# Kernel optimization log

Hardware: AMD Instinct MI355X
Metric: run time of the kernel (lower is better)

Reference implementation:

```python
import jax, jax.numpy as jnp
import numpy as np

B, T, D, H = 128, 64, 1024, 16
HD = D // H  # head dim = 64, matches smolgen per-pair bias last dim


def setup_inputs() -> dict:
    key = jax.random.key(0)
    ks = jax.random.split(key, 8)
    w = 0.02  # RandomNormal(stddev=0.02) init used throughout the repo
    return {
        "x": jax.random.normal(ks[0], (B, T, D), jnp.float32),
        # per-pair smolgen biases, shared across heads: [B, T, T, head_dim]
        "a_q": jax.random.normal(ks[1], (B, T, T, HD), jnp.float32) * 0.1,
        "a_k": jax.random.normal(ks[2], (B, T, T, HD), jnp.float32) * 0.1,
        "a_v": jax.random.normal(ks[3], (B, T, T, HD), jnp.float32) * 0.1,
        "Wq": jax.random.normal(ks[4], (D, D), jnp.float32) * w,
        "Wk": jax.random.normal(ks[5], (D, D), jnp.float32) * w,
        "Wv": jax.random.normal(ks[6], (D, D), jnp.float32) * w,
        "Wo": jax.random.normal(ks[7], (D, D), jnp.float32) * w,
    }


def reference(x, a_q, a_k, a_v, Wq, Wk, Wv, Wo):
    b, t, d_model = x.shape
    q = (x @ Wq).reshape(b, t, H, HD)
    k = (x @ Wk).reshape(b, t, H, HD)
    v = (x @ Wv).reshape(b, t, H, HD)
    scale = 1.0 / np.sqrt(HD).astype(np.float32)
    # standard content-content logits
    logits = jnp.einsum("bqhd,bkhd->bhqk", q, k) * scale
    # additive per-pair smolgen biases folded into QK^T (broadcast over heads)
    logits = logits + jnp.einsum("bqkd,bkhd->bhqk", a_q, k)
    logits = logits + jnp.einsum("bqhd,bqkd->bhqk", q, a_k)
    probs = jax.nn.softmax(logits, axis=-1)
    out = jnp.einsum("bhqk,bkhd->bqhd", probs, v)
    # per-pair value bias gathered by attention weights
    out = out + jnp.einsum("bhqk,bqkd->bqhd", probs, a_v)
    return out.reshape(b, t, d_model) @ Wo
```

## Files before the change

kernel.cpp:

```cpp
#include <hip/hip_runtime.h>
#include <hip/hip_bf16.h>

#define Bn 128
#define Tn 64
#define Dn 1024
#define Hn 16
#define HDn 64

typedef __bf16 bf16_t;
typedef __bf16 bf16x8 __attribute__((ext_vector_type(8)));
typedef float f32x4 __attribute__((ext_vector_type(4)));

__device__ __forceinline__ f32x4 mfma16(bf16x8 a, bf16x8 b, f32x4 c) {
  return __builtin_amdgcn_mfma_f32_16x16x32_bf16(a, b, c, 0, 0, 0);
}

__device__ __forceinline__ bf16x8 ld8f(const float* p) {
  float4 a = *(const float4*)p;
  float4 b = *(const float4*)(p + 4);
  bf16x8 r;
  r[0] = (bf16_t)a.x; r[1] = (bf16_t)a.y; r[2] = (bf16_t)a.z; r[3] = (bf16_t)a.w;
  r[4] = (bf16_t)b.x; r[5] = (bf16_t)b.y; r[6] = (bf16_t)b.z; r[7] = (bf16_t)b.w;
  return r;
}

__global__ __launch_bounds__(256) void convert_bf16(const float* __restrict__ src,
                                                    bf16_t* __restrict__ dst) {
  long i = ((long)blockIdx.x * 256 + threadIdx.x) * 8;
  *(bf16x8*)(dst + i) = ld8f(src + i);
}

__global__ __launch_bounds__(256) void transpose_mat(const float* __restrict__ W,
                                                     bf16_t* __restrict__ Wt) {
  __shared__ bf16_t tile[64][65];
  const int tr = blockIdx.y, tc = blockIdx.x;
  const int t = threadIdx.x;
#pragma unroll
  for (int i = 0; i < 16; i++) {
    int idx = t + i * 256;
    int r = idx >> 6, c = idx & 63;
    tile[r][c] = (bf16_t)W[(long)(tr * 64 + r) * 1024 + tc * 64 + c];
  }
  __syncthreads();
#pragma unroll
  for (int i = 0; i < 16; i++) {
    int idx = t + i * 256;
    int c = idx >> 6, r = idx & 63;
    Wt[(long)(tc * 64 + c) * 1024 + tr * 64 + r] = tile[r][c];
  }
}

template <typename CT>
__global__ __launch_bounds__(256) void gemm_bt(const bf16_t* __restrict__ A,
                                               const bf16_t* __restrict__ Bt,
                                               CT* __restrict__ C,
                                               int M, int N, int K) {
  __shared__ bf16_t As[128 * 64];
  __shared__ bf16_t Bs[128 * 64];
  const int t = threadIdx.x;
  const int w = t >> 6, lane = t & 63;
  const int l16 = lane & 15, quad = lane >> 4;
  const int m0 = blockIdx.y * 128, n0 = blockIdx.x * 128;
  const int wm = (w >> 1) * 64, wn = (w & 1) * 64;

  f32x4 acc[4][4];
#pragma unroll
  for (int i = 0; i < 4; i++)
#pragma unroll
    for (int j = 0; j < 4; j++) acc[i][j] = (f32x4){0.f, 0.f, 0.f, 0.f};

  const int sr = t >> 3;
  const int sc = (t & 7) * 8;

  for (int k0 = 0; k0 < K; k0 += 64) {
    __syncthreads();
#pragma unroll
    for (int i = 0; i < 4; i++) {
      int row = i * 32 + sr;
      *(bf16x8*)(As + row * 64 + sc) =
          *(const bf16x8*)(A + (long)(m0 + row) * K + k0 + sc);
      *(bf16x8*)(Bs + row * 64 + sc) =
          *(const bf16x8*)(Bt + (long)(n0 + row) * K + k0 + sc);
    }
    __syncthreads();
#pragma unroll
    for (int kk = 0; kk < 64; kk += 32) {
      bf16x8 af[4], bfr[4];
#pragma unroll
      for (int i = 0; i < 4; i++)
        af[i] = *(const bf16x8*)(As + (wm + i * 16 + l16) * 64 + kk + quad * 8);
#pragma unroll
      for (int j = 0; j < 4; j++)
        bfr[j] = *(const bf16x8*)(Bs + (wn + j * 16 + l16) * 64 + kk + quad * 8);
#pragma unroll
      for (int i = 0; i < 4; i++)
#pragma unroll
        for (int j = 0; j < 4; j++) acc[i][j] = mfma16(af[i], bfr[j], acc[i][j]);
    }
  }
#pragma unroll
  for (int i = 0; i < 4; i++)
#pragma unroll
    for (int j = 0; j < 4; j++) {
      int col = n0 + wn + j * 16 + l16;
#pragma unroll
      for (int r = 0; r < 4; r++) {
        int row = m0 + wm + i * 16 + quad * 4 + r;
        C[(long)row * N + col] = (CT)acc[i][j][r];
      }
    }
}

__global__ __launch_bounds__(1024) void fused_att(
    const bf16_t* __restrict__ Qb, const bf16_t* __restrict__ Kb,
    const float* __restrict__ aqp, const float* __restrict__ akp,
    const float* __restrict__ avp,
    bf16_t* __restrict__ probs, bf16_t* __restrict__ out2) {
  __shared__ float Ls[256 * 65];
  __shared__ bf16_t Pb[256 * 64];

  const int id = blockIdx.x;
  const int b = (id & 7) * 16 + ((id >> 3) & 15);
  const int q0 = (id >> 7) * 16;
  const int t = threadIdx.x;
  const int w = t >> 6, lane = t & 63, l16 = lane & 15, quad = lane >> 4;

  {
    const int h = w;
    f32x4 acc[4];
#pragma unroll
    for (int j = 0; j < 4; j++) acc[j] = (f32x4){0.f, 0.f, 0.f, 0.f};
    const bf16_t* qb = Qb + (long)(b * Tn + q0 + l16) * Dn + h * HDn;
    const bf16_t* kb = Kb + (long)b * (Tn * Dn) + h * HDn;
#pragma unroll
    for (int kk = 0; kk < 64; kk += 32) {
      bf16x8 af = *(const bf16x8*)(qb + kk + quad * 8);
#pragma unroll
      for (int j = 0; j < 4; j++) {
        bf16x8 bf = *(const bf16x8*)(kb + (long)(j * 16 + l16) * Dn + kk + quad * 8);
        acc[j] = mfma16(af, bf, acc[j]);
      }
    }
#pragma unroll
    for (int j = 0; j < 4; j++)
#pragma unroll
      for (int r = 0; r < 4; r++)
        Ls[((quad * 4 + r) * 16 + h) * 65 + j * 16 + l16] = 0.125f * acc[j][r];
  }
  __syncthreads();

  {
    const float* ab = aqp + (long)(b * Tn + q0 + l16) * (Tn * HDn);
    const bf16_t* kb = Kb + (long)b * (Tn * Dn) + l16 * HDn;
#pragma unroll
    for (int kc = 0; kc < 4; kc++) {
      const int k = w * 4 + kc;
      f32x4 acc = (f32x4){0.f, 0.f, 0.f, 0.f};
#pragma unroll
      for (int kk = 0; kk < 64; kk += 32) {
        bf16x8 af = ld8f(ab + k * HDn + kk + quad * 8);
        bf16x8 bf = *(const bf16x8*)(kb + (long)k * Dn + kk + quad * 8);
        acc = mfma16(af, bf, acc);
      }
#pragma unroll
      for (int r = 0; r < 4; r++)
        Ls[((quad * 4 + r) * 16 + l16) * 65 + k] += acc[r];
    }
  }
  __syncthreads();

  {
    const int q = w;
    const bf16_t* qb = Qb + (long)(b * Tn + q0 + q) * Dn + l16 * HDn;
    const float* ab = akp + (long)(b * Tn + q0 + q) * (Tn * HDn);
    f32x4 acc[4];
#pragma unroll
    for (int j = 0; j < 4; j++) acc[j] = (f32x4){0.f, 0.f, 0.f, 0.f};
#pragma unroll
    for (int kk = 0; kk < 64; kk += 32) {
      bf16x8 af = *(const bf16x8*)(qb + kk + quad * 8);
#pragma unroll
      for (int j = 0; j < 4; j++) {
        bf16x8 bf = ld8f(ab + (long)(j * 16 + l16) * HDn + kk + quad * 8);
        acc[j] = mfma16(af, bf, acc[j]);
      }
    }
#pragma unroll
    for (int j = 0; j < 4; j++)
#pragma unroll
      for (int r = 0; r < 4; r++)
        Ls[(q * 16 + quad * 4 + r) * 65 + j * 16 + l16] += acc[j][r];
  }
  __syncthreads();

  {
    const int r = t >> 2, qq = t & 3;
    const int q = r >> 4, h = r & 15;
    const float* row = Ls + r * 65 + qq * 16;
    float m = -1e30f;
#pragma unroll
    for (int i = 0; i < 16; i++) m = fmaxf(m, row[i]);
    m = fmaxf(m, __shfl_xor(m, 1));
    m = fmaxf(m, __shfl_xor(m, 2));
    float e[16];
    float s = 0.f;
#pragma unroll
    for (int i = 0; i < 16; i++) { e[i] = __expf(row[i] - m); s += e[i]; }
    s += __shfl_xor(s, 1);
    s += __shfl_xor(s, 2);
    const float inv = 1.0f / s;
    const int swz = (q ^ h) & 7;
    bf16_t* pr = probs + ((long)(b * Hn + h) * Tn + q0 + q) * Tn + qq * 16;
#pragma unroll
    for (int c = 0; c < 2; c++) {
      bf16x8 v;
#pragma unroll
      for (int ee = 0; ee < 8; ee++) v[ee] = (bf16_t)(e[c * 8 + ee] * inv);
      *(bf16x8*)(pr + c * 8) = v;
      const int cg = qq * 2 + c;
      *(bf16x8*)(Pb + r * 64 + (cg ^ swz) * 8) = v;
    }
  }

  {
    const int q = w;
    bf16_t* avT = (bf16_t*)(Ls + 16 * w * 65);
    const float* src = avp + (long)(b * Tn + q0 + q) * (Tn * HDn) + lane * HDn;
    f32x4 acc[4];
#pragma unroll
    for (int j = 0; j < 4; j++) acc[j] = (f32x4){0.f, 0.f, 0.f, 0.f};
    const int aswz = (q ^ l16) & 7;
#pragma unroll
    for (int half = 0; half < 2; half++) {
      asm volatile("s_waitcnt lgkmcnt(0)" ::: "memory");
#pragma unroll
      for (int c = 0; c < 8; c++) {
        float4 v = *(const float4*)(src + half * 32 + c * 4);
#pragma unroll
        for (int ee = 0; ee < 4; ee++) {
          int dl = c * 4 + ee;
          avT[dl * 64 + (((lane >> 3) ^ dl) & 7) * 8 + (lane & 7)] =
              (bf16_t)(&v.x)[ee];
        }
      }
      asm volatile("s_waitcnt lgkmcnt(0)" ::: "memory");
      __builtin_amdgcn_sched_barrier(0);
#pragma unroll
      for (int kk = 0; kk < 64; kk += 32) {
        const int cg = (kk >> 3) + quad;
        bf16x8 af = *(const bf16x8*)(Pb + (q * 16 + l16) * 64 + (cg ^ aswz) * 8);
#pragma unroll
        for (int jj = 0; jj < 2; jj++) {
          int j = half * 2 + jj;
          int dl = jj * 16 + l16;
          bf16x8 bf = *(const bf16x8*)(avT + dl * 64 + ((cg ^ (dl & 7))) * 8);
          acc[j] = mfma16(af, bf, acc[j]);
        }
      }
    }
    bf16_t* ob = out2 + (long)(b * Tn + q0 + q) * Dn;
#pragma unroll
    for (int j = 0; j < 4; j++)
#pragma unroll
      for (int r = 0; r < 4; r++)
        ob[(quad * 4 + r) * HDn + j * 16 + l16] = (bf16_t)acc[j][r];
  }
}

__global__ __launch_bounds__(256) void pv_out(const bf16_t* __restrict__ probs,
                                              const bf16_t* __restrict__ V,
                                              const bf16_t* __restrict__ out2,
                                              bf16_t* __restrict__ attn) {
  const int h = blockIdx.x, b = blockIdx.y;
  __shared__ bf16_t VT[64][72];
  const int t = threadIdx.x, w = t >> 6, lane = t & 63;
  const int l16 = lane & 15, quad = lane >> 4;

  {
    const bf16_t* src = V + (long)b * (Tn * Dn) + h * HDn;
    int k = t & 63, d0 = (t >> 6) * 16;
    union { uint4 u; unsigned short s[8]; } v0, v1;
    v0.u = *(const uint4*)(src + (long)k * Dn + d0);
    v1.u = *(const uint4*)(src + (long)k * Dn + d0 + 8);
    unsigned short* lds = (unsigned short*)&VT[0][0];
#pragma unroll
    for (int j = 0; j < 8; j++) lds[(d0 + j) * 72 + k] = v0.s[j];
#pragma unroll
    for (int j = 0; j < 8; j++) lds[(d0 + 8 + j) * 72 + k] = v1.s[j];
  }
  __syncthreads();

  const bf16_t* pbase = probs + ((long)(b * Hn + h) * Tn) * Tn;
  f32x4 acc[4];
#pragma unroll
  for (int j = 0; j < 4; j++) acc[j] = (f32x4){0.f, 0.f, 0.f, 0.f};
#pragma unroll
  for (int kk = 0; kk < 64; kk += 32) {
    bf16x8 af = *(const bf16x8*)(pbase + (long)(w * 16 + l16) * Tn + kk + quad * 8);
#pragma unroll
    for (int j = 0; j < 4; j++) {
      bf16x8 bfr = *(const bf16x8*)(&VT[j * 16 + l16][kk + quad * 8]);
      acc[j] = mfma16(af, bfr, acc[j]);
    }
  }
#pragma unroll
  for (int j = 0; j < 4; j++)
#pragma unroll
    for (int r = 0; r < 4; r++) {
      int qrow = w * 16 + quad * 4 + r, d = j * 16 + l16;
      long idx = (long)(b * Tn + qrow) * Dn + h * HDn + d;
      attn[idx] = (bf16_t)(acc[j][r] + (float)out2[idx]);
    }
}

extern "C" void kernel_launch(void* const* d_in, const int* in_sizes, int n_in,
                              void* d_out, int out_size, void* d_ws, size_t ws_size,
                              hipStream_t stream) {
  const float* x  = (const float*)d_in[0];
  const float* aq = (const float*)d_in[1];
  const float* ak = (const float*)d_in[2];
  const float* av = (const float*)d_in[3];
  const float* Wq = (const float*)d_in[4];
  const float* Wk = (const float*)d_in[5];
  const float* Wv = (const float*)d_in[6];
  const float* Wo = (const float*)d_in[7];
  float* out = (float*)d_out;

  char* ws = (char*)d_ws;
  const size_t MB = 1024 * 1024;
  bf16_t* WqT    = (bf16_t*)(ws + 0 * MB);
  bf16_t* WkT    = (bf16_t*)(ws + 2 * MB);
  bf16_t* WvT    = (bf16_t*)(ws + 4 * MB);
  bf16_t* WoT    = (bf16_t*)(ws + 6 * MB);
  bf16_t* xb     = (bf16_t*)(ws + 8 * MB);
  bf16_t* Qb     = (bf16_t*)(ws + 24 * MB);
  bf16_t* Kb     = (bf16_t*)(ws + 40 * MB);
  bf16_t* Vb     = (bf16_t*)(ws + 56 * MB);
  bf16_t* probs  = (bf16_t*)(ws + 72 * MB);
  bf16_t* out2   = (bf16_t*)(ws + 88 * MB);
  bf16_t* attn   = (bf16_t*)(ws + 104 * MB);

  dim3 blk(256);
  convert_bf16<<<dim3(4096), blk, 0, stream>>>(x, xb);
  transpose_mat<<<dim3(16, 16), blk, 0, stream>>>(Wq, WqT);
  transpose_mat<<<dim3(16, 16), blk, 0, stream>>>(Wk, WkT);
  transpose_mat<<<dim3(16, 16), blk, 0, stream>>>(Wv, WvT);
  transpose_mat<<<dim3(16, 16), blk, 0, stream>>>(Wo, WoT);

  gemm_bt<bf16_t><<<dim3(8, 64), blk, 0, stream>>>(xb, WqT, Qb, Bn * Tn, Dn, Dn);
  gemm_bt<bf16_t><<<dim3(8, 64), blk, 0, stream>>>(xb, WkT, Kb, Bn * Tn, Dn, Dn);
  gemm_bt<bf16_t><<<dim3(8, 64), blk, 0, stream>>>(xb, WvT, Vb, Bn * Tn, Dn, Dn);

  fused_att<<<dim3(512), dim3(1024), 0, stream>>>(Qb, Kb, aq, ak, av, probs, out2);

  pv_out<<<dim3(Hn, Bn), blk, 0, stream>>>(probs, Vb, out2, attn);

  gemm_bt<float><<<dim3(8, 64), blk, 0, stream>>>(attn, WoT, out, Bn * Tn, Dn, Dn);
}
```

Baseline: 577.9 us.

## Alias attention probs into logits LDS and use direct global-to-LDS GEMM loads

The fused attention kernel drops its separate shared bf16 probability buffer. Each wave now writes its softmax outputs as bf16 into the start of its own float logits rows. It then holds the A-operand fragments in registers before reusing the same LDS region for the transposed value-bias tile. This cuts shared memory per block so more blocks can be resident, and adds a launch-bounds occupancy hint. The GEMM staging loop also switches to global_load_lds so tiles go straight to LDS without passing through registers, at the cost of relying on per-wave contiguous LDS placement and in-wave ordering for correctness.

```diff
diff --git a/kernel.cpp b/kernel.cpp
--- a/kernel.cpp
+++ b/kernel.cpp
@@ -22,6 +22,12 @@
   r[0] = (bf16_t)a.x; r[1] = (bf16_t)a.y; r[2] = (bf16_t)a.z; r[3] = (bf16_t)a.w;
   r[4] = (bf16_t)b.x; r[5] = (bf16_t)b.y; r[6] = (bf16_t)b.z; r[7] = (bf16_t)b.w;
   return r;
+}
+
+__device__ __forceinline__ void gload16(const bf16_t* g, bf16_t* l) {
+  __builtin_amdgcn_global_load_lds(
+      (const __attribute__((address_space(1))) void*)g,
+      (__attribute__((address_space(3))) void*)l, 16, 0, 0);
 }
 
 __global__ __launch_bounds__(256) void convert_bf16(const float* __restrict__ src,
@@ -76,11 +82,8 @@
     __syncthreads();
 #pragma unroll
     for (int i = 0; i < 4; i++) {
-      int row = i * 32 + sr;
-      *(bf16x8*)(As + row * 64 + sc) =
-          *(const bf16x8*)(A + (long)(m0 + row) * K + k0 + sc);
-      *(bf16x8*)(Bs + row * 64 + sc) =
-          *(const bf16x8*)(Bt + (long)(n0 + row) * K + k0 + sc);
+      gload16(A + (long)(m0 + i * 32 + sr) * K + k0 + sc, As + (i * 32 + w * 8) * 64);
+      gload16(Bt + (long)(n0 + i * 32 + sr) * K + k0 + sc, Bs + (i * 32 + w * 8) * 64);
     }
     __syncthreads();
 #pragma unroll
@@ -111,13 +114,12 @@
     }
 }
 
-__global__ __launch_bounds__(1024) void fused_att(
+__global__ __launch_bounds__(1024, 8) void fused_att(
     const bf16_t* __restrict__ Qb, const bf16_t* __restrict__ Kb,
     const float* __restrict__ aqp, const float* __restrict__ akp,
     const float* __restrict__ avp,
     bf16_t* __restrict__ probs, bf16_t* __restrict__ out2) {
   __shared__ float Ls[256 * 65];
-  __shared__ bf16_t Pb[256 * 64];
 
   const int id = blockIdx.x;
   const int b = (id & 7) * 16 + ((id >> 3) & 15);
@@ -195,60 +197,65 @@
 
   {
     const int r = t >> 2, qq = t & 3;
-    const int q = r >> 4, h = r & 15;
-    const float* row = Ls + r * 65 + qq * 16;
-    float m = -1e30f;
-#pragma unroll
-    for (int i = 0; i < 16; i++) m = fmaxf(m, row[i]);
+    const float* rowf = Ls + r * 65 + qq * 16;
+    float v[16];
+#pragma unroll
+    for (int i = 0; i < 16; i++) v[i] = rowf[i];
+    float m = v[0];
+#pragma unroll
+    for (int i = 1; i < 16; i++) m = fmaxf(m, v[i]);
     m = fmaxf(m, __shfl_xor(m, 1));
     m = fmaxf(m, __shfl_xor(m, 2));
-    float e[16];
     float s = 0.f;
 #pragma unroll
-    for (int i = 0; i < 16; i++) { e[i] = __expf(row[i] - m); s += e[i]; }
+    for (int i = 0; i < 16; i++) { v[i] = __expf(v[i] - m); s += v[i]; }
     s += __shfl_xor(s, 1);
     s += __shfl_xor(s, 2);
     const float inv = 1.0f / s;
-    const int swz = (q ^ h) & 7;
-    bf16_t* pr = probs + ((long)(b * Hn + h) * Tn + q0 + q) * Tn + qq * 16;
+    const int q = r >> 4, h = r & 15;
+    bf16_t* prow = (bf16_t*)(Ls + r * 65) + qq * 16;
+    bf16_t* pg = probs + ((long)(b * Hn + h) * Tn + q0 + q) * Tn + qq * 16;
 #pragma unroll
     for (int c = 0; c < 2; c++) {
-      bf16x8 v;
-#pragma unroll
-      for (int ee = 0; ee < 8; ee++) v[ee] = (bf16_t)(e[c * 8 + ee] * inv);
-      *(bf16x8*)(pr + c * 8) = v;
-      const int cg = qq * 2 + c;
-      *(bf16x8*)(Pb + r * 64 + (cg ^ swz) * 8) = v;
+      bf16x8 pv8;
+#pragma unroll
+      for (int ee = 0; ee < 8; ee++) pv8[ee] = (bf16_t)(v[c * 8 + ee] * inv);
+      *(bf16x8*)(pg + c * 8) = pv8;
+      *(bf16x8*)(prow + c * 8) = pv8;
     }
   }
 
   {
     const int q = w;
+    const bf16_t* prow = (const bf16_t*)(Ls + (q * 16 + l16) * 65);
+    bf16x8 paf0 = *(const bf16x8*)(prow + quad * 8);
+    bf16x8 paf1 = *(const bf16x8*)(prow + 32 + quad * 8);
+    asm volatile("s_waitcnt lgkmcnt(0)" ::: "memory");
+    __builtin_amdgcn_sched_barrier(0);
+
     bf16_t* avT = (bf16_t*)(Ls + 16 * w * 65);
     const float* src = avp + (long)(b * Tn + q0 + q) * (Tn * HDn) + lane * HDn;
     f32x4 acc[4];
 #pragma unroll
     for (int j = 0; j < 4; j++) acc[j] = (f32x4){0.f, 0.f, 0.f, 0.f};
-    const int aswz = (q ^ l16) & 7;
 #pragma unroll
     for (int half = 0; half < 2; half++) {
-      asm volatile("s_waitcnt lgkmcnt(0)" ::: "memory");
 #pragma unroll
       for (int c = 0; c < 8; c++) {
-        float4 v = *(const float4*)(src + half * 32 + c * 4);
+        float4 vv = *(const float4*)(src + half * 32 + c * 4);
 #pragma unroll
         for (int ee = 0; ee < 4; ee++) {
           int dl = c * 4 + ee;
           avT[dl * 64 + (((lane >> 3) ^ dl) & 7) * 8 + (lane & 7)] =
-              (bf16_t)(&v.x)[ee];
+              (bf16_t)(&vv.x)[ee];
         }
       }
       asm volatile("s_waitcnt lgkmcnt(0)" ::: "memory");
       __builtin_amdgcn_sched_barrier(0);
 #pragma unroll
       for (int kk = 0; kk < 64; kk += 32) {
+        bf16x8 af = (kk == 0) ? paf0 : paf1;
         const int cg = (kk >> 3) + quad;
-        bf16x8 af = *(const bf16x8*)(Pb + (q * 16 + l16) * 64 + (cg ^ aswz) * 8);
 #pragma unroll
         for (int jj = 0; jj < 2; jj++) {
           int j = half * 2 + jj;
@@ -256,6 +263,10 @@
           bf16x8 bf = *(const bf16x8*)(avT + dl * 64 + ((cg ^ (dl & 7))) * 8);
           acc[j] = mfma16(af, bf, acc[j]);
         }
+      }
+      if (half == 0) {
+        asm volatile("s_waitcnt lgkmcnt(0)" ::: "memory");
+        __builtin_amdgcn_sched_barrier(0);
       }
     }
     bf16_t* ob = out2 + (long)(b * Tn + q0 + q) * Dn;
```

After: 566.3 us. 2.0% less time.
